# Kernel optimization log

Hardware: AMD Instinct MI355X
Metric: run time of the kernel (lower is better)

The kernel has to match this reference:

```python
import jax, jax.numpy as jnp
import numpy as np


def setup_inputs() -> dict:
    key = jax.random.key(0)
    k1, k2, k3, k4 = jax.random.split(key, 4)
    N, E, IN, OUT = 100000, 1600000, 256, 32
    feat = jax.random.normal(k1, (N, IN), dtype=jnp.float32)
    src = jax.random.randint(k2, (E,), 0, N, dtype=jnp.int64)
    dst = jax.random.randint(k3, (E,), 0, N, dtype=jnp.int64)
    weight = jax.random.normal(k4, (IN, OUT), dtype=jnp.float32) * (6.0 / (IN + OUT)) ** 0.5
    bias = jnp.zeros((OUT,), dtype=jnp.float32)
    return {"feat": feat, "src": src, "dst": dst, "weight": weight, "bias": bias}


def reference(feat, src, dst, weight, bias):
    N = feat.shape[0]
    ones = jnp.ones(src.shape[0], dtype=feat.dtype)
    # norm='both': scale sources by out_degree^-0.5
    out_deg = jnp.clip(jax.ops.segment_sum(ones, src, num_segments=N), 1.0)
    feat = feat * (out_deg ** -0.5)[:, None]
    # in_feats (256) > out_feats (32): apply weight before aggregation
    feat = feat @ weight
    # SpMM: copy_src + sum over destination nodes
    rst = jax.ops.segment_sum(feat[src], dst, num_segments=N)  # [N, out]
    # scale destinations by in_degree^-0.5
    in_deg = jnp.clip(jax.ops.segment_sum(ones, dst, num_segments=N), 1.0)
    rst = rst * (in_deg ** -0.5)[:, None]
    rst = rst + bias
    return jax.nn.relu(rst)
```

## Files before the change

### kernel.cpp

```cpp
#include <hip/hip_runtime.h>
#include <hip/hip_bf16.h>


#define IN_F 256
#define OUT_F 32

#define G_ROWS 128
#define G_BK 16
#define W_ROWS 32
#define G_NT (IN_F / G_BK)

#define BSHIFT 7
#define BNODES 128
#define NBK 1024
#define PB_EDGES 8192
#define AGG_CAP 4096


__global__ __launch_bounds__(1024) void hist_kernel(
    const int* __restrict__ src, const int* __restrict__ dst,
    unsigned short* __restrict__ mhistS, unsigned short* __restrict__ mhistD,
    int E) {
  __shared__ int hS[NBK], hD[NBK];
  int tid = threadIdx.x;
  hS[tid] = 0; hD[tid] = 0;
  __syncthreads();
  int e0 = blockIdx.x * PB_EDGES + tid * 8;
  if (e0 + 8 <= E) {
    int4 a0 = ((const int4*)(src + e0))[0], a1 = ((const int4*)(src + e0))[1];
    int4 b0 = ((const int4*)(dst + e0))[0], b1 = ((const int4*)(dst + e0))[1];
    int ss[8] = {a0.x, a0.y, a0.z, a0.w, a1.x, a1.y, a1.z, a1.w};
    int dd[8] = {b0.x, b0.y, b0.z, b0.w, b1.x, b1.y, b1.z, b1.w};
#pragma unroll
    for (int j = 0; j < 8; ++j) {
      atomicAdd(&hS[ss[j] >> BSHIFT], 1);
      atomicAdd(&hD[dd[j] >> BSHIFT], 1);
    }
  } else {
    for (int j = 0; j < 8; ++j) {
      int e = e0 + j;
      if (e < E) {
        atomicAdd(&hS[src[e] >> BSHIFT], 1);
        atomicAdd(&hD[dst[e] >> BSHIFT], 1);
      }
    }
  }
  __syncthreads();
  mhistS[blockIdx.x * NBK + tid] = (unsigned short)hS[tid];
  mhistD[blockIdx.x * NBK + tid] = (unsigned short)hD[tid];
}

__global__ __launch_bounds__(1024) void offset_kernel(
    unsigned short* __restrict__ mhistS, unsigned short* __restrict__ mhistD,
    int* __restrict__ baseS, int* __restrict__ baseD, int npb) {
  __shared__ int wsum[16];
  unsigned short* mh = blockIdx.x ? mhistD : mhistS;
  int* bb = blockIdx.x ? baseD : baseS;
  int b = threadIdx.x;
  int run = 0;
  int blk = 0;
  for (; blk + 4 <= npb; blk += 4) {
    int i0 = blk * NBK + b;
    int c0 = mh[i0];
    int c1 = mh[i0 + NBK];
    int c2 = mh[i0 + 2 * NBK];
    int c3 = mh[i0 + 3 * NBK];
    mh[i0] = (unsigned short)run;
    mh[i0 + NBK] = (unsigned short)(run + c0);
    mh[i0 + 2 * NBK] = (unsigned short)(run + c0 + c1);
    mh[i0 + 3 * NBK] = (unsigned short)(run + c0 + c1 + c2);
    run += c0 + c1 + c2 + c3;
  }
  for (; blk < npb; ++blk) {
    int idx = blk * NBK + b;
    int c = mh[idx];
    mh[idx] = (unsigned short)run;
    run += c;
  }
  int v = run, x = run;
#pragma unroll
  for (int d = 1; d < 64; d <<= 1) {
    int y = __shfl_up(x, d, 64);
    if ((b & 63) >= d) x += y;
  }
  if ((b & 63) == 63) wsum[b >> 6] = x;
  __syncthreads();
  int off = 0;
#pragma unroll
  for (int w = 0; w < 16; ++w)
    if (w < (b >> 6)) off += wsum[w];
  bb[b] = off + x - v;
  if (b == NBK - 1) bb[NBK] = off + x;
}

__global__ __launch_bounds__(1024) void partition_src_kernel(
    const int* __restrict__ src, const unsigned short* __restrict__ mbaseS,
    const int* __restrict__ baseS, unsigned char* __restrict__ pairs_s, int E) {
  __shared__ unsigned char sbuf[PB_EDGES];
  __shared__ int hist[NBK];
  __shared__ int lbase[NBK + 1];
  __shared__ int gbase[NBK];
  __shared__ int wsum[16];

  int tid = threadIdx.x;
  hist[tid] = 0;
  __syncthreads();

  int e0 = blockIdx.x * PB_EDGES + tid * 8;
  int myb[8], myslot[8];
  unsigned char mylow[8];
  if (e0 + 8 <= E) {
    int4 a0 = ((const int4*)(src + e0))[0], a1 = ((const int4*)(src + e0))[1];
    int ss[8] = {a0.x, a0.y, a0.z, a0.w, a1.x, a1.y, a1.z, a1.w};
#pragma unroll
    for (int j = 0; j < 8; ++j) {
      int b = ss[j] >> BSHIFT;
      myb[j] = b;
      mylow[j] = (unsigned char)(ss[j] & (BNODES - 1));
      myslot[j] = atomicAdd(&hist[b], 1);
    }
  } else {
#pragma unroll
    for (int j = 0; j < 8; ++j) {
      int e = e0 + j;
      if (e < E) {
        int s = src[e];
        int b = s >> BSHIFT;
        myb[j] = b;
        mylow[j] = (unsigned char)(s & (BNODES - 1));
        myslot[j] = atomicAdd(&hist[b], 1);
      } else {
        myb[j] = -1;
      }
    }
  }
  __syncthreads();

  {
    int v = hist[tid];
    int x = v;
#pragma unroll
    for (int d = 1; d < 64; d <<= 1) {
      int y = __shfl_up(x, d, 64);
      if ((tid & 63) >= d) x += y;
    }
    if ((tid & 63) == 63) wsum[tid >> 6] = x;
    __syncthreads();
    int off = 0;
#pragma unroll
    for (int w = 0; w < 16; ++w)
      if (w < (tid >> 6)) off += wsum[w];
    lbase[tid] = off + x - v;
    if (tid == NBK - 1) lbase[NBK] = off + x;
    gbase[tid] = baseS[tid] + (int)mbaseS[blockIdx.x * NBK + tid];
  }
  __syncthreads();

#pragma unroll
  for (int j = 0; j < 8; ++j)
    if (myb[j] >= 0) sbuf[lbase[myb[j]] + myslot[j]] = mylow[j];
  __syncthreads();

  int total = lbase[NBK];
  int idx = tid * 8;
  if (idx < total) {
    int lo = 0, hi = NBK;
    while (hi - lo > 1) {
      int mid = (lo + hi) >> 1;
      if (lbase[mid] <= idx) lo = mid; else hi = mid;
    }
    int b = lo;
#pragma unroll
    for (int j = 0; j < 8; ++j, ++idx) {
      if (idx >= total) break;
      while (idx >= lbase[b + 1]) ++b;
      pairs_s[gbase[b] + (idx - lbase[b])] = sbuf[idx];
    }
  }
}

__global__ __launch_bounds__(256) void src_count_kernel(
    const unsigned char* __restrict__ pairs_s, const int* __restrict__ baseS,
    float* __restrict__ scale_out, int N) {
  __shared__ int hist[BNODES];
  int tid = threadIdx.x;
  int b = blockIdx.x;
  if (tid < BNODES) hist[tid] = 0;
  __syncthreads();
  int s = baseS[b], e = baseS[b + 1];
  for (int i = s + tid; i < e; i += 256) atomicAdd(&hist[pairs_s[i]], 1);
  __syncthreads();
  if (tid < BNODES) {
    int node = (b << BSHIFT) + tid;
    if (node < N) {
      int c = hist[tid];
      scale_out[node] = (c < 1) ? 1.f : rsqrtf((float)c);
    }
  }
}

__global__ __launch_bounds__(256, 4) void gemm_kernel(
    const float* __restrict__ feat, const float* __restrict__ W,
    const float* __restrict__ scale_out, float* __restrict__ h, int N) {
  __shared__ float sW[IN_F * OUT_F];
  __shared__ float sF[4][2][W_ROWS * G_BK];
  __shared__ float sScale[G_ROWS];

  int tid = threadIdx.x;
  int wv = tid >> 6;
  int lane = tid & 63;
  {
    const float4* W4 = (const float4*)W;
    float4* sW4 = (float4*)sW;
#pragma unroll
    for (int i = 0; i < 8; ++i) sW4[tid + i * 256] = W4[tid + i * 256];
  }
  int grow = blockIdx.x * G_ROWS;
  if (tid < G_ROWS) {
    int gr = grow + tid;
    sScale[tid] = (gr < N) ? scale_out[gr] : 0.f;
  }
  int wrow0 = grow + wv * W_ROWS;

  auto stage = [&](int t) {
    int k0 = t * G_BK;
    float* dstb = &sF[wv][t & 1][0];
#pragma unroll
    for (int q = 0; q < 2; ++q) {
      int r = q * 16 + (lane >> 2);
      int c = (lane & 3) ^ (r & 3);
      int g = wrow0 + r;
      if (g >= N) g = N - 1;
      const float* gp = feat + (size_t)g * IN_F + k0 + c * 4;
      __builtin_amdgcn_global_load_lds(
          (const __attribute__((address_space(1))) unsigned int*)gp,
          (__attribute__((address_space(3))) unsigned int*)(dstb + q * 256 + lane * 4),
          16, 0, 0);
    }
  };

  stage(0);

  int tr = lane >> 3;
  int cg = (lane & 7) * 4;

  float acc[4][4];
#pragma unroll
  for (int i = 0; i < 4; ++i)
#pragma unroll
    for (int c = 0; c < 4; ++c) acc[i][c] = 0.f;

  __syncthreads();

  for (int t = 0; t < G_NT; ++t) {
    if (t + 1 < G_NT) {
      stage(t + 1);
      asm volatile("s_waitcnt vmcnt(2)" ::: "memory");
    } else {
      asm volatile("s_waitcnt vmcnt(0)" ::: "memory");
    }

    const float* sf = &sF[wv][t & 1][0];
    int kb = t * G_BK;
#pragma unroll
    for (int cc = 0; cc < 4; ++cc) {
      float4 a[4];
#pragma unroll
      for (int i = 0; i < 4; ++i) {
        int r = tr + 8 * i;
        a[i] = *(const float4*)(sf + r * 16 + ((cc ^ (r & 3)) << 2));
      }
#pragma unroll
      for (int j = 0; j < 4; ++j) {
        float4 w = *(const float4*)(sW + (kb + cc * 4 + j) * OUT_F + cg);
#pragma unroll
        for (int i = 0; i < 4; ++i) {
          float aj = (j == 0) ? a[i].x : (j == 1) ? a[i].y
                   : (j == 2) ? a[i].z : a[i].w;
          acc[i][0] = fmaf(aj, w.x, acc[i][0]);
          acc[i][1] = fmaf(aj, w.y, acc[i][1]);
          acc[i][2] = fmaf(aj, w.z, acc[i][2]);
          acc[i][3] = fmaf(aj, w.w, acc[i][3]);
        }
      }
    }
  }

#pragma unroll
  for (int i = 0; i < 4; ++i) {
    int r = tr + 8 * i;
    int g = wrow0 + r;
    if (g < N) {
      float s = sScale[wv * W_ROWS + r];
      float4 o = {acc[i][0] * s, acc[i][1] * s, acc[i][2] * s, acc[i][3] * s};
      *(float4*)(h + (size_t)g * OUT_F + cg) = o;
    }
  }
}

__global__ __launch_bounds__(1024) void partition_dst_kernel(
    const int* __restrict__ src, const int* __restrict__ dst,
    const unsigned short* __restrict__ mbaseD, const int* __restrict__ baseD,
    unsigned* __restrict__ pairs, int E) {
  __shared__ unsigned sbuf[PB_EDGES];
  __shared__ int hist[NBK];
  __shared__ int lbase[NBK + 1];
  __shared__ int gbase[NBK];
  __shared__ int wsum[16];

  int tid = threadIdx.x;
  hist[tid] = 0;
  __syncthreads();

  int e0 = blockIdx.x * PB_EDGES + tid * 8;
  int myb[8], myslot[8];
  unsigned mypk[8];
  if (e0 + 8 <= E) {
    int4 a0 = ((const int4*)(src + e0))[0], a1 = ((const int4*)(src + e0))[1];
    int4 b0 = ((const int4*)(dst + e0))[0], b1 = ((const int4*)(dst + e0))[1];
    int ss[8] = {a0.x, a0.y, a0.z, a0.w, a1.x, a1.y, a1.z, a1.w};
    int dd[8] = {b0.x, b0.y, b0.z, b0.w, b1.x, b1.y, b1.z, b1.w};
#pragma unroll
    for (int j = 0; j < 8; ++j) {
      int b = dd[j] >> BSHIFT;
      myb[j] = b;
      mypk[j] = (unsigned)ss[j] | ((unsigned)(dd[j] & (BNODES - 1)) << 17);
      myslot[j] = atomicAdd(&hist[b], 1);
    }
  } else {
#pragma unroll
    for (int j = 0; j < 8; ++j) {
      int e = e0 + j;
      if (e < E) {
        int s = src[e], d = dst[e];
        int b = d >> BSHIFT;
        myb[j] = b;
        mypk[j] = (unsigned)s | ((unsigned)(d & (BNODES - 1)) << 17);
        myslot[j] = atomicAdd(&hist[b], 1);
      } else {
        myb[j] = -1;
      }
    }
  }
  __syncthreads();

  {
    int v = hist[tid];
    int x = v;
#pragma unroll
    for (int d = 1; d < 64; d <<= 1) {
      int y = __shfl_up(x, d, 64);
      if ((tid & 63) >= d) x += y;
    }
    if ((tid & 63) == 63) wsum[tid >> 6] = x;
    __syncthreads();
    int off = 0;
#pragma unroll
    for (int w = 0; w < 16; ++w)
      if (w < (tid >> 6)) off += wsum[w];
    lbase[tid] = off + x - v;
    if (tid == NBK - 1) lbase[NBK] = off + x;
    gbase[tid] = baseD[tid] + (int)mbaseD[blockIdx.x * NBK + tid];
  }
  __syncthreads();

#pragma unroll
  for (int j = 0; j < 8; ++j)
    if (myb[j] >= 0) sbuf[lbase[myb[j]] + myslot[j]] = mypk[j];
  __syncthreads();

  int total = lbase[NBK];
  int idx = tid * 8;
  if (idx < total) {
    int lo = 0, hi = NBK;
    while (hi - lo > 1) {
      int mid = (lo + hi) >> 1;
      if (lbase[mid] <= idx) lo = mid; else hi = mid;
    }
    int b = lo;
#pragma unroll
    for (int j = 0; j < 8; ++j, ++idx) {
      if (idx >= total) break;
      while (idx >= lbase[b + 1]) ++b;
      pairs[gbase[b] + (idx - lbase[b])] = sbuf[idx];
    }
  }
}

__global__ __launch_bounds__(256) void sort_agg_kernel(
    const unsigned* __restrict__ pairs, const int* __restrict__ baseD,
    const float* __restrict__ h, const float* __restrict__ bias,
    float* __restrict__ out, int N) {
  __shared__ unsigned spk[AGG_CAP];
  __shared__ int hist[BNODES];
  __shared__ int rs[BNODES + 1];
  __shared__ int wsum2[4];

  int tid = threadIdx.x;
  int lane = tid & 31;
  int eg = tid >> 5;
  int b = blockIdx.x;
  int start = baseD[b];
  int end = baseD[b + 1];

  float acc[16];
  int degc[16];
#pragma unroll
  for (int t = 0; t < 16; ++t) { acc[t] = 0.f; degc[t] = 0; }

  for (int chunk = start; chunk < end; chunk += AGG_CAP) {
    int cnt = min(end - chunk, AGG_CAP);
    if (tid < BNODES) hist[tid] = 0;
    __syncthreads();

    unsigned mypk[16];
    int myslot[16];
    int nmine = 0;
    for (int i = tid; i < cnt; i += 256) {
      unsigned pk = pairs[chunk + i];
      mypk[nmine] = pk;
      myslot[nmine] = atomicAdd(&hist[pk >> 17], 1);
      ++nmine;
    }
    __syncthreads();

    {
      int v = (tid < BNODES) ? hist[tid] : 0;
      int x = v;
#pragma unroll
      for (int d = 1; d < 64; d <<= 1) {
        int y = __shfl_up(x, d, 64);
        if ((tid & 63) >= d) x += y;
      }
      if ((tid & 63) == 63) wsum2[tid >> 6] = x;
      __syncthreads();
      int off = (tid >= 64 && tid < BNODES) ? wsum2[0] : 0;
      if (tid < BNODES) rs[tid] = off + x - v;
      if (tid == BNODES - 1) rs[BNODES] = off + x;
    }
    __syncthreads();

    for (int i = 0; i < nmine; ++i) {
      unsigned pk = mypk[i];
      spk[rs[pk >> 17] + myslot[i]] = pk;
    }
    __syncthreads();

#pragma unroll 1
    for (int t = 0; t < 16; ++t) {
      int n = eg * 16 + t;
      int a = rs[n], bnd = rs[n + 1];
      degc[t] += bnd - a;
      float s = acc[t];
      int j = a;
      for (; j + 8 <= bnd; j += 8) {
        unsigned p0 = spk[j], p1 = spk[j + 1], p2 = spk[j + 2], p3 = spk[j + 3];
        unsigned p4 = spk[j + 4], p5 = spk[j + 5], p6 = spk[j + 6], p7 = spk[j + 7];
        float f0 = h[(size_t)(p0 & 0x1FFFF) * OUT_F + lane];
        float f1 = h[(size_t)(p1 & 0x1FFFF) * OUT_F + lane];
        float f2 = h[(size_t)(p2 & 0x1FFFF) * OUT_F + lane];
        float f3 = h[(size_t)(p3 & 0x1FFFF) * OUT_F + lane];
        float f4 = h[(size_t)(p4 & 0x1FFFF) * OUT_F + lane];
        float f5 = h[(size_t)(p5 & 0x1FFFF) * OUT_F + lane];
        float f6 = h[(size_t)(p6 & 0x1FFFF) * OUT_F + lane];
        float f7 = h[(size_t)(p7 & 0x1FFFF) * OUT_F + lane];
        s += ((f0 + f1) + (f2 + f3)) + ((f4 + f5) + (f6 + f7));
      }
      if (j + 4 <= bnd) {
        unsigned p0 = spk[j], p1 = spk[j + 1], p2 = spk[j + 2], p3 = spk[j + 3];
        float f0 = h[(size_t)(p0 & 0x1FFFF) * OUT_F + lane];
        float f1 = h[(size_t)(p1 & 0x1FFFF) * OUT_F + lane];
        float f2 = h[(size_t)(p2 & 0x1FFFF) * OUT_F + lane];
        float f3 = h[(size_t)(p3 & 0x1FFFF) * OUT_F + lane];
        s += (f0 + f1) + (f2 + f3);
        j += 4;
      }
      for (; j < bnd; ++j)
        s += h[(size_t)(spk[j] & 0x1FFFF) * OUT_F + lane];
      acc[t] = s;
    }
    __syncthreads();
  }

  int node0 = b << BSHIFT;
#pragma unroll
  for (int t = 0; t < 16; ++t) {
    int node = node0 + eg * 16 + t;
    if (node < N) {
      float sc = degc[t] > 0 ? rsqrtf((float)degc[t]) : 1.f;
      out[(size_t)node * OUT_F + lane] = fmaxf(fmaf(acc[t], sc, bias[lane]), 0.f);
    }
  }
}

__global__ __launch_bounds__(256) void degree_kernel(
    const int* __restrict__ src, const int* __restrict__ dst,
    int* __restrict__ cnt_out, int* __restrict__ cnt_in, int E) {
  int i = blockIdx.x * 256 + threadIdx.x;
  if (i < E) {
    atomicAdd(cnt_out + src[i], 1);
    atomicAdd(cnt_in + dst[i], 1);
  }
}

__global__ __launch_bounds__(256) void cnt_to_scale_kernel(
    const int* __restrict__ cnt, float* __restrict__ scale, int N) {
  int i = blockIdx.x * 256 + threadIdx.x;
  if (i < N) {
    int c = cnt[i];
    scale[i] = (c < 1) ? 1.f : rsqrtf((float)c);
  }
}

__global__ __launch_bounds__(256) void aggregate_kernel(
    const int* __restrict__ src, const int* __restrict__ dst,
    const float* __restrict__ h, float* __restrict__ out, int E) {
  int lane = threadIdx.x & 31;
  int e = (blockIdx.x * 256 + threadIdx.x) >> 5;
  if (e >= E) return;
  float v = h[(size_t)src[e] * OUT_F + lane];
  unsafeAtomicAdd(out + (size_t)dst[e] * OUT_F + lane, v);
}

__global__ __launch_bounds__(256) void finalize_kernel(
    float* __restrict__ out, const int* __restrict__ cnt_in,
    const float* __restrict__ bias, int N) {
  int idx = blockIdx.x * 256 + threadIdx.x;
  if (idx >= N * 8) return;
  int n = idx >> 3;
  int o = (idx & 7) * 4;
  float dg = (float)cnt_in[n];
  float s = dg < 1.f ? 1.f : rsqrtf(dg);
  float4 bv = *(const float4*)(bias + o);
  float4 v = ((const float4*)out)[idx];
  v.x = fmaxf(fmaf(v.x, s, bv.x), 0.f);
  v.y = fmaxf(fmaf(v.y, s, bv.y), 0.f);
  v.z = fmaxf(fmaf(v.z, s, bv.z), 0.f);
  v.w = fmaxf(fmaf(v.w, s, bv.w), 0.f);
  ((float4*)out)[idx] = v;
}

extern "C" void kernel_launch(void* const* d_in, const int* in_sizes, int n_in,
                              void* d_out, int out_size, void* d_ws, size_t ws_size,
                              hipStream_t stream) {
  const float* feat = (const float*)d_in[0];
  const int* src = (const int*)d_in[1];
  const int* dst = (const int*)d_in[2];
  const float* weight = (const float*)d_in[3];
  const float* bias = (const float*)d_in[4];
  float* out = (float*)d_out;

  int N = in_sizes[0] / IN_F;
  int E = in_sizes[1];
  int nb = (N + BNODES - 1) >> BSHIFT;
  int npb = (E + PB_EDGES - 1) / PB_EDGES;

  float* h = (float*)d_ws;
  unsigned* pairs = (unsigned*)(h + (size_t)N * OUT_F);
  unsigned char* pairs_s = (unsigned char*)pairs;
  unsigned short* mhistS = (unsigned short*)(pairs + E);
  unsigned short* mhistD = mhistS + (size_t)npb * NBK;
  int* baseS = (int*)(mhistD + (size_t)npb * NBK);
  int* baseD = baseS + NBK + 1;
  float* scale_out = (float*)(baseD + NBK + 1);

  size_t need = ((size_t)N * OUT_F + (size_t)E + (size_t)N + 2 * (NBK + 1)) * 4 +
                (size_t)npb * NBK * 2 * 2;
  bool fast = (ws_size >= need) && (N <= (1 << 17)) && (nb <= NBK);

  if (fast) {
    hist_kernel<<<npb, 1024, 0, stream>>>(src, dst, mhistS, mhistD, E);
    offset_kernel<<<2, 1024, 0, stream>>>(mhistS, mhistD, baseS, baseD, npb);
    partition_src_kernel<<<npb, 1024, 0, stream>>>(src, mhistS, baseS, pairs_s, E);
    src_count_kernel<<<nb, 256, 0, stream>>>(pairs_s, baseS, scale_out, N);
    gemm_kernel<<<(N + G_ROWS - 1) / G_ROWS, 256, 0, stream>>>(
        feat, weight, scale_out, h, N);
    partition_dst_kernel<<<npb, 1024, 0, stream>>>(src, dst, mhistD, baseD, pairs, E);
    sort_agg_kernel<<<nb, 256, 0, stream>>>(pairs, baseD, h, bias, out, N);
  } else {
    int* cnt_out = (int*)(h + (size_t)N * OUT_F);
    int* cnt_in = cnt_out + N;
    float* scl = (float*)(cnt_in + N);
    hipMemsetAsync(cnt_out, 0, (size_t)2 * N * sizeof(int), stream);
    hipMemsetAsync(out, 0, (size_t)N * OUT_F * sizeof(float), stream);
    degree_kernel<<<(E + 255) / 256, 256, 0, stream>>>(src, dst, cnt_out, cnt_in, E);
    cnt_to_scale_kernel<<<(N + 255) / 256, 256, 0, stream>>>(cnt_out, scl, N);
    gemm_kernel<<<(N + G_ROWS - 1) / G_ROWS, 256, 0, stream>>>(feat, weight, scl, h, N);
    aggregate_kernel<<<(E + 7) / 8, 256, 0, stream>>>(src, dst, h, out, E);
    finalize_kernel<<<(N * 8 + 255) / 256, 256, 0, stream>>>(out, cnt_in, bias, N);
  }
}
```

Before: 279.6 us.

## Parallelize bucket offset scan and fuse src/dst partition kernels

The serial per-bucket offset scan, which ran on two blocks looping over all partition blocks, is split into a wave-per-bucket parallel scan plus a small base-scan kernel. The source and destination partition passes are merged into one launch with twice as many blocks, and pairs_s gets its own buffer so both can run at once. Edges per partition block are halved, which doubles the block count and raises parallelism. The cost is an extra launch, larger histogram arrays, and the dst partition now running before the GEMM rather than after it.

```diff
diff --git a/kernel.cpp b/kernel.cpp
--- a/kernel.cpp
+++ b/kernel.cpp
@@ -13,7 +13,7 @@
 #define BSHIFT 7
 #define BNODES 128
 #define NBK 1024
-#define PB_EDGES 8192
+#define PB_EDGES 4096
 #define AGG_CAP 4096
 
 
@@ -25,19 +25,19 @@
   int tid = threadIdx.x;
   hS[tid] = 0; hD[tid] = 0;
   __syncthreads();
-  int e0 = blockIdx.x * PB_EDGES + tid * 8;
-  if (e0 + 8 <= E) {
-    int4 a0 = ((const int4*)(src + e0))[0], a1 = ((const int4*)(src + e0))[1];
-    int4 b0 = ((const int4*)(dst + e0))[0], b1 = ((const int4*)(dst + e0))[1];
-    int ss[8] = {a0.x, a0.y, a0.z, a0.w, a1.x, a1.y, a1.z, a1.w};
-    int dd[8] = {b0.x, b0.y, b0.z, b0.w, b1.x, b1.y, b1.z, b1.w};
-#pragma unroll
-    for (int j = 0; j < 8; ++j) {
+  int e0 = blockIdx.x * PB_EDGES + tid * 4;
+  if (e0 + 4 <= E) {
+    int4 a0 = *(const int4*)(src + e0);
+    int4 b0 = *(const int4*)(dst + e0);
+    int ss[4] = {a0.x, a0.y, a0.z, a0.w};
+    int dd[4] = {b0.x, b0.y, b0.z, b0.w};
+#pragma unroll
+    for (int j = 0; j < 4; ++j) {
       atomicAdd(&hS[ss[j] >> BSHIFT], 1);
       atomicAdd(&hD[dd[j] >> BSHIFT], 1);
     }
   } else {
-    for (int j = 0; j < 8; ++j) {
+    for (int j = 0; j < 4; ++j) {
       int e = e0 + j;
       if (e < E) {
         atomicAdd(&hS[src[e] >> BSHIFT], 1);
@@ -50,34 +50,40 @@
   mhistD[blockIdx.x * NBK + tid] = (unsigned short)hD[tid];
 }
 
-__global__ __launch_bounds__(1024) void offset_kernel(
+__global__ __launch_bounds__(256) void offset_bucket_kernel(
     unsigned short* __restrict__ mhistS, unsigned short* __restrict__ mhistD,
-    int* __restrict__ baseS, int* __restrict__ baseD, int npb) {
+    int* __restrict__ totS, int* __restrict__ totD, int npb) {
+  int gid = blockIdx.x * 4 + (threadIdx.x >> 6);
+  int lane = threadIdx.x & 63;
+  int a = gid >> 10;
+  int b = gid & (NBK - 1);
+  unsigned short* mh = a ? mhistD : mhistS;
+  int* tot = a ? totD : totS;
+  int carry = 0;
+  for (int c0 = 0; c0 < npb; c0 += 64) {
+    int idx = c0 + lane;
+    int v = (idx < npb) ? (int)mh[(size_t)idx * NBK + b] : 0;
+    int x = v;
+#pragma unroll
+    for (int d = 1; d < 64; d <<= 1) {
+      int y = __shfl_up(x, d, 64);
+      if (lane >= d) x += y;
+    }
+    if (idx < npb) mh[(size_t)idx * NBK + b] = (unsigned short)(carry + x - v);
+    carry += __shfl(x, 63, 64);
+  }
+  if (lane == 0) tot[b] = carry;
+}
+
+__global__ __launch_bounds__(1024) void offset_base_kernel(
+    const int* __restrict__ totS, const int* __restrict__ totD,
+    int* __restrict__ baseS, int* __restrict__ baseD) {
   __shared__ int wsum[16];
-  unsigned short* mh = blockIdx.x ? mhistD : mhistS;
+  const int* tt = blockIdx.x ? totD : totS;
   int* bb = blockIdx.x ? baseD : baseS;
   int b = threadIdx.x;
-  int run = 0;
-  int blk = 0;
-  for (; blk + 4 <= npb; blk += 4) {
-    int i0 = blk * NBK + b;
-    int c0 = mh[i0];
-    int c1 = mh[i0 + NBK];
-    int c2 = mh[i0 + 2 * NBK];
-    int c3 = mh[i0 + 3 * NBK];
-    mh[i0] = (unsigned short)run;
-    mh[i0 + NBK] = (unsigned short)(run + c0);
-    mh[i0 + 2 * NBK] = (unsigned short)(run + c0 + c1);
-    mh[i0 + 3 * NBK] = (unsigned short)(run + c0 + c1 + c2);
-    run += c0 + c1 + c2 + c3;
-  }
-  for (; blk < npb; ++blk) {
-    int idx = blk * NBK + b;
-    int c = mh[idx];
-    mh[idx] = (unsigned short)run;
-    run += c;
-  }
-  int v = run, x = run;
+  int v = tt[b];
+  int x = v;
 #pragma unroll
   for (int d = 1; d < 64; d <<= 1) {
     int y = __shfl_up(x, d, 64);
@@ -93,44 +99,81 @@
   if (b == NBK - 1) bb[NBK] = off + x;
 }
 
-__global__ __launch_bounds__(1024) void partition_src_kernel(
-    const int* __restrict__ src, const unsigned short* __restrict__ mbaseS,
-    const int* __restrict__ baseS, unsigned char* __restrict__ pairs_s, int E) {
-  __shared__ unsigned char sbuf[PB_EDGES];
+__global__ __launch_bounds__(1024) void partition_fused_kernel(
+    const int* __restrict__ src, const int* __restrict__ dst,
+    const unsigned short* __restrict__ mbaseS,
+    const unsigned short* __restrict__ mbaseD,
+    const int* __restrict__ baseS, const int* __restrict__ baseD,
+    unsigned char* __restrict__ pairs_s, unsigned* __restrict__ pairs,
+    int E, int npb) {
+  __shared__ unsigned sbuf[PB_EDGES];
   __shared__ int hist[NBK];
   __shared__ int lbase[NBK + 1];
   __shared__ int gbase[NBK];
   __shared__ int wsum[16];
 
   int tid = threadIdx.x;
+  bool isDst = (int)blockIdx.x >= npb;
+  int pb = isDst ? (int)blockIdx.x - npb : (int)blockIdx.x;
   hist[tid] = 0;
   __syncthreads();
 
-  int e0 = blockIdx.x * PB_EDGES + tid * 8;
-  int myb[8], myslot[8];
-  unsigned char mylow[8];
-  if (e0 + 8 <= E) {
-    int4 a0 = ((const int4*)(src + e0))[0], a1 = ((const int4*)(src + e0))[1];
-    int ss[8] = {a0.x, a0.y, a0.z, a0.w, a1.x, a1.y, a1.z, a1.w};
-#pragma unroll
-    for (int j = 0; j < 8; ++j) {
-      int b = ss[j] >> BSHIFT;
-      myb[j] = b;
-      mylow[j] = (unsigned char)(ss[j] & (BNODES - 1));
-      myslot[j] = atomicAdd(&hist[b], 1);
+  int e0 = pb * PB_EDGES + tid * 4;
+  int myb[4], myslot[4];
+  unsigned mypk[4];
+  unsigned char mylow[4];
+  if (!isDst) {
+    if (e0 + 4 <= E) {
+      int4 a0 = *(const int4*)(src + e0);
+      int ss[4] = {a0.x, a0.y, a0.z, a0.w};
+#pragma unroll
+      for (int j = 0; j < 4; ++j) {
+        int b = ss[j] >> BSHIFT;
+        myb[j] = b;
+        mylow[j] = (unsigned char)(ss[j] & (BNODES - 1));
+        myslot[j] = atomicAdd(&hist[b], 1);
+      }
+    } else {
+#pragma unroll
+      for (int j = 0; j < 4; ++j) {
+        int e = e0 + j;
+        if (e < E) {
+          int s = src[e];
+          int b = s >> BSHIFT;
+          myb[j] = b;
+          mylow[j] = (unsigned char)(s & (BNODES - 1));
+          myslot[j] = atomicAdd(&hist[b], 1);
+        } else {
+          myb[j] = -1;
+        }
+      }
     }
   } else {
-#pragma unroll
-    for (int j = 0; j < 8; ++j) {
-      int e = e0 + j;
-      if (e < E) {
-        int s = src[e];
-        int b = s >> BSHIFT;
+    if (e0 + 4 <= E) {
+      int4 a0 = *(const int4*)(src + e0);
+      int4 b0 = *(const int4*)(dst + e0);
+      int ss[4] = {a0.x, a0.y, a0.z, a0.w};
+      int dd[4] = {b0.x, b0.y, b0.z, b0.w};
+#pragma unroll
+      for (int j = 0; j < 4; ++j) {
+        int b = dd[j] >> BSHIFT;
         myb[j] = b;
-        mylow[j] = (unsigned char)(s & (BNODES - 1));
+        mypk[j] = (unsigned)ss[j] | ((unsigned)(dd[j] & (BNODES - 1)) << 17);
         myslot[j] = atomicAdd(&hist[b], 1);
-      } else {
-        myb[j] = -1;
+      }
+    } else {
+#pragma unroll
+      for (int j = 0; j < 4; ++j) {
+        int e = e0 + j;
+        if (e < E) {
+          int s = src[e], d = dst[e];
+          int b = d >> BSHIFT;
+          myb[j] = b;
+          mypk[j] = (unsigned)s | ((unsigned)(d & (BNODES - 1)) << 17);
+          myslot[j] = atomicAdd(&hist[b], 1);
+        } else {
+          myb[j] = -1;
+        }
       }
     }
   }
@@ -152,17 +195,27 @@
       if (w < (tid >> 6)) off += wsum[w];
     lbase[tid] = off + x - v;
     if (tid == NBK - 1) lbase[NBK] = off + x;
-    gbase[tid] = baseS[tid] + (int)mbaseS[blockIdx.x * NBK + tid];
-  }
-  __syncthreads();
-
-#pragma unroll
-  for (int j = 0; j < 8; ++j)
-    if (myb[j] >= 0) sbuf[lbase[myb[j]] + myslot[j]] = mylow[j];
+    if (isDst)
+      gbase[tid] = baseD[tid] + (int)mbaseD[(size_t)pb * NBK + tid];
+    else
+      gbase[tid] = baseS[tid] + (int)mbaseS[(size_t)pb * NBK + tid];
+  }
+  __syncthreads();
+
+  if (!isDst) {
+    unsigned char* sbuf8 = (unsigned char*)sbuf;
+#pragma unroll
+    for (int j = 0; j < 4; ++j)
+      if (myb[j] >= 0) sbuf8[lbase[myb[j]] + myslot[j]] = mylow[j];
+  } else {
+#pragma unroll
+    for (int j = 0; j < 4; ++j)
+      if (myb[j] >= 0) sbuf[lbase[myb[j]] + myslot[j]] = mypk[j];
+  }
   __syncthreads();
 
   int total = lbase[NBK];
-  int idx = tid * 8;
+  int idx = tid * 4;
   if (idx < total) {
     int lo = 0, hi = NBK;
     while (hi - lo > 1) {
@@ -170,11 +223,21 @@
       if (lbase[mid] <= idx) lo = mid; else hi = mid;
     }
     int b = lo;
-#pragma unroll
-    for (int j = 0; j < 8; ++j, ++idx) {
-      if (idx >= total) break;
-      while (idx >= lbase[b + 1]) ++b;
-      pairs_s[gbase[b] + (idx - lbase[b])] = sbuf[idx];
+    if (!isDst) {
+      unsigned char* sbuf8 = (unsigned char*)sbuf;
+#pragma unroll
+      for (int j = 0; j < 4; ++j, ++idx) {
+        if (idx >= total) break;
+        while (idx >= lbase[b + 1]) ++b;
+        pairs_s[gbase[b] + (idx - lbase[b])] = sbuf8[idx];
+      }
+    } else {
+#pragma unroll
+      for (int j = 0; j < 4; ++j, ++idx) {
+        if (idx >= total) break;
+        while (idx >= lbase[b + 1]) ++b;
+        pairs[gbase[b] + (idx - lbase[b])] = sbuf[idx];
+      }
     }
   }
 }
@@ -294,95 +357,6 @@
       float s = sScale[wv * W_ROWS + r];
       float4 o = {acc[i][0] * s, acc[i][1] * s, acc[i][2] * s, acc[i][3] * s};
       *(float4*)(h + (size_t)g * OUT_F + cg) = o;
-    }
-  }
-}
-
-__global__ __launch_bounds__(1024) void partition_dst_kernel(
-    const int* __restrict__ src, const int* __restrict__ dst,
-    const unsigned short* __restrict__ mbaseD, const int* __restrict__ baseD,
-    unsigned* __restrict__ pairs, int E) {
-  __shared__ unsigned sbuf[PB_EDGES];
-  __shared__ int hist[NBK];
-  __shared__ int lbase[NBK + 1];
-  __shared__ int gbase[NBK];
-  __shared__ int wsum[16];
-
-  int tid = threadIdx.x;
-  hist[tid] = 0;
-  __syncthreads();
-
-  int e0 = blockIdx.x * PB_EDGES + tid * 8;
-  int myb[8], myslot[8];
-  unsigned mypk[8];
-  if (e0 + 8 <= E) {
-    int4 a0 = ((const int4*)(src + e0))[0], a1 = ((const int4*)(src + e0))[1];
-    int4 b0 = ((const int4*)(dst + e0))[0], b1 = ((const int4*)(dst + e0))[1];
-    int ss[8] = {a0.x, a0.y, a0.z, a0.w, a1.x, a1.y, a1.z, a1.w};
-    int dd[8] = {b0.x, b0.y, b0.z, b0.w, b1.x, b1.y, b1.z, b1.w};
-#pragma unroll
-    for (int j = 0; j < 8; ++j) {
-      int b = dd[j] >> BSHIFT;
-      myb[j] = b;
-      mypk[j] = (unsigned)ss[j] | ((unsigned)(dd[j] & (BNODES - 1)) << 17);
-      myslot[j] = atomicAdd(&hist[b], 1);
-    }
-  } else {
-#pragma unroll
-    for (int j = 0; j < 8; ++j) {
-      int e = e0 + j;
-      if (e < E) {
-        int s = src[e], d = dst[e];
-        int b = d >> BSHIFT;
-        myb[j] = b;
-        mypk[j] = (unsigned)s | ((unsigned)(d & (BNODES - 1)) << 17);
-        myslot[j] = atomicAdd(&hist[b], 1);
-      } else {
-        myb[j] = -1;
-      }
-    }
-  }
-  __syncthreads();
-
-  {
-    int v = hist[tid];
-    int x = v;
-#pragma unroll
-    for (int d = 1; d < 64; d <<= 1) {
-      int y = __shfl_up(x, d, 64);
-      if ((tid & 63) >= d) x += y;
-    }
-    if ((tid & 63) == 63) wsum[tid >> 6] = x;
-    __syncthreads();
-    int off = 0;
-#pragma unroll
-    for (int w = 0; w < 16; ++w)
-      if (w < (tid >> 6)) off += wsum[w];
-    lbase[tid] = off + x - v;
-    if (tid == NBK - 1) lbase[NBK] = off + x;
-    gbase[tid] = baseD[tid] + (int)mbaseD[blockIdx.x * NBK + tid];
-  }
-  __syncthreads();
-
-#pragma unroll
-  for (int j = 0; j < 8; ++j)
-    if (myb[j] >= 0) sbuf[lbase[myb[j]] + myslot[j]] = mypk[j];
-  __syncthreads();
-
-  int total = lbase[NBK];
-  int idx = tid * 8;
-  if (idx < total) {
-    int lo = 0, hi = NBK;
-    while (hi - lo > 1) {
-      int mid = (lo + hi) >> 1;
-      if (lbase[mid] <= idx) lo = mid; else hi = mid;
-    }
-    int b = lo;
-#pragma unroll
-    for (int j = 0; j < 8; ++j, ++idx) {
-      if (idx >= total) break;
-      while (idx >= lbase[b + 1]) ++b;
-      pairs[gbase[b] + (idx - lbase[b])] = sbuf[idx];
     }
   }
 }
@@ -558,24 +532,31 @@
   float* h = (float*)d_ws;
   unsigned* pairs = (unsigned*)(h + (size_t)N * OUT_F);
   unsigned char* pairs_s = (unsigned char*)pairs;
-  unsigned short* mhistS = (unsigned short*)(pairs + E);
+  pairs_s = (unsigned char*)(pairs + E);
+  unsigned short* mhistS =
+      (unsigned short*)(pairs_s + ((size_t)E + 3 & ~(size_t)3));
   unsigned short* mhistD = mhistS + (size_t)npb * NBK;
   int* baseS = (int*)(mhistD + (size_t)npb * NBK);
   int* baseD = baseS + NBK + 1;
-  float* scale_out = (float*)(baseD + NBK + 1);
-
-  size_t need = ((size_t)N * OUT_F + (size_t)E + (size_t)N + 2 * (NBK + 1)) * 4 +
-                (size_t)npb * NBK * 2 * 2;
+  int* totS = baseD + NBK + 1;
+  int* totD = totS + NBK;
+  float* scale_out = (float*)(totD + NBK);
+
+  size_t need = ((size_t)N * OUT_F + (size_t)E + (size_t)N +
+                 2 * (NBK + 1) + 2 * NBK) * 4 +
+                (size_t)E + (size_t)npb * NBK * 2 * 2 + 16;
   bool fast = (ws_size >= need) && (N <= (1 << 17)) && (nb <= NBK);
 
   if (fast) {
     hist_kernel<<<npb, 1024, 0, stream>>>(src, dst, mhistS, mhistD, E);
-    offset_kernel<<<2, 1024, 0, stream>>>(mhistS, mhistD, baseS, baseD, npb);
-    partition_src_kernel<<<npb, 1024, 0, stream>>>(src, mhistS, baseS, pairs_s, E);
+    offset_bucket_kernel<<<2 * NBK / 4, 256, 0, stream>>>(
+        mhistS, mhistD, totS, totD, npb);
+    offset_base_kernel<<<2, 1024, 0, stream>>>(totS, totD, baseS, baseD);
+    partition_fused_kernel<<<2 * npb, 1024, 0, stream>>>(
+        src, dst, mhistS, mhistD, baseS, baseD, pairs_s, pairs, E, npb);
     src_count_kernel<<<nb, 256, 0, stream>>>(pairs_s, baseS, scale_out, N);
     gemm_kernel<<<(N + G_ROWS - 1) / G_ROWS, 256, 0, stream>>>(
         feat, weight, scale_out, h, N);
-    partition_dst_kernel<<<npb, 1024, 0, stream>>>(src, dst, mhistD, baseD, pairs, E);
     sort_agg_kernel<<<nb, 256, 0, stream>>>(pairs, baseD, h, bias, out, N);
   } else {
     int* cnt_out = (int*)(h + (size_t)N * OUT_F);
```

Measured after the change: 272.5 us. 1.03x faster.
